# Kernel optimization log

Hardware: AMD Instinct MI355X
Metric: run time of the kernel (lower is better)

Reference implementation:

```python
import jax, jax.numpy as jnp
import numpy as np

NUM_FEATURES = 26
H1 = 24
H2 = 8
SEQ_LEN = 5
BATCH = 262144


def _lstm(x, w_ih, w_hh, b_ih, b_hh):
    """batch_first LSTM matching torch gate order (i, f, g, o).
    x: [B, T, I]; w_ih: [4H, I]; w_hh: [4H, H]; b_*: [4H].
    Returns (outputs [B, T, H], h_final [B, H])."""
    H = w_hh.shape[1]
    B = x.shape[0]
    # Precompute input contribution for all timesteps: [T, B, 4H]
    xg = jnp.einsum('bti,gi->tbg', x, w_ih) + (b_ih + b_hh)

    def step(carry, g_t):
        h, c = carry
        gates = g_t + h @ w_hh.T  # [B, 4H]
        i, f, g, o = jnp.split(gates, 4, axis=-1)
        i = jax.nn.sigmoid(i)
        f = jax.nn.sigmoid(f)
        g = jnp.tanh(g)
        o = jax.nn.sigmoid(o)
        c = f * c + i * g
        h = o * jnp.tanh(c)
        return (h, c), h

    h0 = jnp.zeros((B, H), dtype=x.dtype)
    c0 = jnp.zeros((B, H), dtype=x.dtype)
    (h_final, _), hs = jax.lax.scan(step, (h0, c0), xg)
    return jnp.transpose(hs, (1, 0, 2)), h_final


def setup_inputs() -> dict:
    key = jax.random.key(0)
    ks = jax.random.split(key, 9)
    s1 = 1.0 / np.sqrt(H1)
    s2 = 1.0 / np.sqrt(H2)
    u = lambda k, shape, s: jax.random.uniform(k, shape, jnp.float32, -s, s)
    return {
        'x': jax.random.normal(ks[0], (BATCH, SEQ_LEN, NUM_FEATURES), jnp.float32),
        'w_ih1': u(ks[1], (4 * H1, NUM_FEATURES), s1),
        'w_hh1': u(ks[2], (4 * H1, H1), s1),
        'b_ih1': u(ks[3], (4 * H1,), s1),
        'b_hh1': u(ks[4], (4 * H1,), s1),
        'w_ih2': u(ks[5], (4 * H2, H1), s2),
        'w_hh2': u(ks[6], (4 * H2, H2), s2),
        'b_ih2': u(ks[7], (4 * H2,), s2),
        'b_hh2': u(ks[8], (4 * H2,), s2),
    }


def reference(x, w_ih1, w_hh1, b_ih1, b_hh1, w_ih2, w_hh2, b_ih2, b_hh2):
    y1, _ = _lstm(x, w_ih1, w_hh1, b_ih1, b_hh1)        # [B, T, 24]
    _, h2 = _lstm(y1, w_ih2, w_hh2, b_ih2, b_hh2)        # [B, 8]
    return h2.reshape(-1, 1, H2)                          # [B, 1, 8]
```

## Files before the change

### kernel.cpp

```cpp
#include <hip/hip_runtime.h>

#define DEV_INLINE __device__ __forceinline__

constexpr int NF = 26;
constexpr int H1 = 24;
constexpr int H2 = 8;
constexpr int T  = 5;
constexpr int BPW  = 32;
constexpr int ROWU = 20;

constexpr float L2E     = 1.44269504088896f;
constexpr float TWO_L2E = 2.88539008177792f;

typedef _Float16 f16x8 __attribute__((ext_vector_type(8)));
typedef float    f32x4 __attribute__((ext_vector_type(4)));
typedef __fp16   fp16x2 __attribute__((ext_vector_type(2)));

union Q { uint4 u; f16x8 h; };

DEV_INLINE float fast_rcp(float x) { return __builtin_amdgcn_rcpf(x); }
DEV_INLINE float rcp1p(float x) { return fast_rcp(1.0f + __builtin_amdgcn_exp2f(-x)); }
DEV_INLINE float cellp(float i_, float f_, float g_, float o_, float& c) {
    const float ig = rcp1p(i_), fg = rcp1p(f_);
    const float gg = fmaf(2.0f, rcp1p(g_), -1.0f);
    const float og = rcp1p(o_);
    c = fmaf(fg, c, ig * gg);
    return og * fmaf(2.0f, rcp1p(c * TWO_L2E), -1.0f);
}
DEV_INLINE uint pkrtz(float a, float b) {
    union { uint u; fp16x2 p; } v; v.p = __builtin_amdgcn_cvt_pkrtz(a, b); return v.u;
}
DEV_INLINE float swz8(float v) {
    union { float f; int i; } a, b;
    a.f = v;
    b.i = __builtin_amdgcn_ds_swizzle(a.i, 0x201F);
    return b.f;
}


__global__ __launch_bounds__(256, 5) void lstm2_mfma(
    const float* __restrict__ x,
    const float* __restrict__ w_ih1, const float* __restrict__ w_hh1,
    const float* __restrict__ b_ih1, const float* __restrict__ b_hh1,
    const float* __restrict__ w_ih2, const float* __restrict__ w_hh2,
    const float* __restrict__ b_ih2, const float* __restrict__ b_hh2,
    float* __restrict__ out, int batch)
{
    __shared__ uint4 sW[20][64];
    __shared__ uint  sH[4][BPW * ROWU];
    __shared__ float sB1[8 * 16];
    __shared__ float sB2[4 * 16];

    const int tid = threadIdx.x;
    const int w   = tid >> 6;
    const int l   = tid & 63;
    const int q   = l >> 4;
    const int r16 = l & 15;
    const bool lo = (r16 < 8);
    const int wb  = blockIdx.x * 128 + w * BPW;

    for (int i = l; i < BPW * ROWU; i += 64) sH[w][i] = 0u;

    int row0 = wb + r16;      if (row0 > batch - 1) row0 = batch - 1;
    int row1 = wb + 16 + r16; if (row1 > batch - 1) row1 = batch - 1;
    const float* __restrict__ xp0 = x + (size_t)row0 * (T * NF) + q * 8;
    const float* __restrict__ xp1 = x + (size_t)row1 * (T * NF) + q * 8;
    const bool q3 = (q == 3);
    const float2 z2 = make_float2(0.0f, 0.0f);

    float2 xr_[2][4];
    #pragma unroll
    for (int m = 0; m < 2; ++m) {
        const float* __restrict__ p = m ? xp1 : xp0;
        xr_[m][0] = *reinterpret_cast<const float2*>(p);
        xr_[m][1] = q3 ? z2 : *reinterpret_cast<const float2*>(p + 2);
        xr_[m][2] = q3 ? z2 : *reinterpret_cast<const float2*>(p + 4);
        xr_[m][3] = q3 ? z2 : *reinterpret_cast<const float2*>(p + 6);
    }

    for (int tile = w; tile < 20; tile += 4) {
        f16x8 bf;
        if (tile < 16) {
            const int tau  = tile & 7;
            const int gate = tau >> 1, j = (tau & 1) * 16 + r16;
            const bool jv  = (j < H1);
            const int row  = gate * H1 + (jv ? j : 0);
            const bool ih  = (tile < 8);
            const float sc = (gate == 2) ? TWO_L2E : L2E;
            #pragma unroll
            for (int e = 0; e < 8; ++e) {
                const int k = q * 8 + e;
                float v = 0.0f;
                if (ih) { if (jv && k < NF) v = w_ih1[row * NF + k]; }
                else    { if (jv && k < H1) v = w_hh1[row * H1 + k]; }
                bf[e] = (_Float16)(v * sc);
            }
        } else {
            const int t2  = tile - 16;
            const bool jv = (r16 < H2);
            const int row = t2 * H2 + (jv ? r16 : 0);
            const float sc = (t2 == 2) ? TWO_L2E : L2E;
            #pragma unroll
            for (int e = 0; e < 8; ++e) {
                const int k = q * 8 + e;
                float v = 0.0f;
                if (jv) v = (k < H1) ? w_ih2[row * H1 + k] : w_hh2[row * H2 + (k - H1)];
                bf[e] = (_Float16)(v * sc);
            }
        }
        Q u; u.h = bf;
        sW[tile][l] = u.u;
    }

    if (tid < 128) {
        const int tau = tid >> 4, col = tid & 15;
        const int gate = tau >> 1, j = (tau & 1) * 16 + col;
        const bool jv = (j < H1);
        const int row = gate * H1 + (jv ? j : 0);
        const float sc = (gate == 2) ? TWO_L2E : L2E;
        sB1[tid] = jv ? (b_ih1[row] + b_hh1[row]) * sc : 0.0f;
    } else if (tid < 192) {
        const int idx = tid - 128;
        const int t2 = idx >> 4, col = idx & 15;
        const bool jv = (col < H2);
        const int row = t2 * H2 + (jv ? col : 0);
        const float sc = (t2 == 2) ? TWO_L2E : L2E;
        sB2[idx] = jv ? (b_ih2[row] + b_hh2[row]) * sc : 0.0f;
    }

    __syncthreads();

    float c1a[2][4] = {}, c1b[4] = {}, c2s[4] = {};
    const uint4* HQ = reinterpret_cast<const uint4*>(&sH[w][0]);
    _Float16*   Hh  = reinterpret_cast<_Float16*>(&sH[w][0]);

    #pragma unroll 1
    for (int t = 0; t < T; ++t) {
        Q xa[2];
        #pragma unroll
        for (int m = 0; m < 2; ++m) {
            uint4 u;
            u.x = pkrtz(xr_[m][0].x, xr_[m][0].y);
            u.y = pkrtz(xr_[m][1].x, xr_[m][1].y);
            u.z = pkrtz(xr_[m][2].x, xr_[m][2].y);
            u.w = pkrtz(xr_[m][3].x, xr_[m][3].y);
            xa[m].u = u;
        }
        if (t < T - 1) {
            #pragma unroll
            for (int m = 0; m < 2; ++m) {
                const float* __restrict__ p = (m ? xp1 : xp0) + (t + 1) * NF;
                xr_[m][0] = *reinterpret_cast<const float2*>(p);
                xr_[m][1] = q3 ? z2 : *reinterpret_cast<const float2*>(p + 2);
                xr_[m][2] = q3 ? z2 : *reinterpret_cast<const float2*>(p + 4);
                xr_[m][3] = q3 ? z2 : *reinterpret_cast<const float2*>(p + 6);
            }
        }

        Q ha[2];
        #pragma unroll
        for (int m = 0; m < 2; ++m) ha[m].u = HQ[(m * 16 + r16) * 5 + q];
        __builtin_amdgcn_sched_barrier(0);

        f32x4 acc[2][4];

        #pragma unroll
        for (int g = 0; g < 4; ++g) {
            const float b = sB1[(2 * g) * 16 + r16];
            f32x4 bv = {b, b, b, b};
            acc[0][g] = bv;
            acc[1][g] = bv;
        }
        #pragma unroll
        for (int g = 0; g < 4; ++g) {
            const int tau = 2 * g;
            Q wi, wh;
            wi.u = sW[tau][l];
            wh.u = sW[8 + tau][l];
            acc[0][g] = __builtin_amdgcn_mfma_f32_16x16x32_f16(xa[0].h, wi.h, acc[0][g], 0, 0, 0);
            acc[1][g] = __builtin_amdgcn_mfma_f32_16x16x32_f16(xa[1].h, wi.h, acc[1][g], 0, 0, 0);
            acc[0][g] = __builtin_amdgcn_mfma_f32_16x16x32_f16(ha[0].h, wh.h, acc[0][g], 0, 0, 0);
            acc[1][g] = __builtin_amdgcn_mfma_f32_16x16x32_f16(ha[1].h, wh.h, acc[1][g], 0, 0, 0);
            if (g == 1) __builtin_amdgcn_sched_barrier(0);
        }
        __builtin_amdgcn_sched_barrier(0);
        #pragma unroll
        for (int m = 0; m < 2; ++m) {
            #pragma unroll
            for (int r = 0; r < 4; ++r) {
                const int lrow = m * 16 + q * 4 + r;
                const float hv = cellp(acc[m][0][r], acc[m][1][r], acc[m][2][r], acc[m][3][r], c1a[m][r]);
                Hh[lrow * 40 + r16] = (_Float16)hv;
            }
        }
        __builtin_amdgcn_sched_barrier(0);

        #pragma unroll
        for (int g = 0; g < 4; ++g) {
            const float b = sB1[(2 * g + 1) * 16 + r16];
            f32x4 bv = {b, b, b, b};
            acc[0][g] = bv;
            acc[1][g] = bv;
        }
        #pragma unroll
        for (int g = 0; g < 4; ++g) {
            const int tau = 2 * g + 1;
            Q wi, wh;
            wi.u = sW[tau][l];
            wh.u = sW[8 + tau][l];
            acc[0][g] = __builtin_amdgcn_mfma_f32_16x16x32_f16(xa[0].h, wi.h, acc[0][g], 0, 0, 0);
            acc[1][g] = __builtin_amdgcn_mfma_f32_16x16x32_f16(xa[1].h, wi.h, acc[1][g], 0, 0, 0);
            acc[0][g] = __builtin_amdgcn_mfma_f32_16x16x32_f16(ha[0].h, wh.h, acc[0][g], 0, 0, 0);
            acc[1][g] = __builtin_amdgcn_mfma_f32_16x16x32_f16(ha[1].h, wh.h, acc[1][g], 0, 0, 0);
            if (g == 1) __builtin_amdgcn_sched_barrier(0);
        }
        __builtin_amdgcn_sched_barrier(0);
        #pragma unroll
        for (int r = 0; r < 4; ++r) {
            const float si = swz8(acc[1][0][r]);
            const float sf = swz8(acc[1][1][r]);
            const float sg = swz8(acc[1][2][r]);
            const float so = swz8(acc[1][3][r]);
            const float i_ = lo ? acc[0][0][r] : si;
            const float f_ = lo ? acc[0][1][r] : sf;
            const float g_ = lo ? acc[0][2][r] : sg;
            const float o_ = lo ? acc[0][3][r] : so;
            const float hv = cellp(i_, f_, g_, o_, c1b[r]);
            const int lrow = (lo ? 0 : 16) + q * 4 + r;
            Hh[lrow * 40 + 16 + (r16 & 7)] = (_Float16)hv;
        }
        __builtin_amdgcn_sched_barrier(0);

        Q hc[2];
        #pragma unroll
        for (int m = 0; m < 2; ++m) hc[m].u = HQ[(m * 16 + r16) * 5 + q];
        __builtin_amdgcn_sched_barrier(0);
        #pragma unroll
        for (int t2 = 0; t2 < 4; ++t2) {
            const float b = sB2[t2 * 16 + r16];
            f32x4 bv = {b, b, b, b};
            acc[0][t2] = bv;
            acc[1][t2] = bv;
        }
        #pragma unroll
        for (int t2 = 0; t2 < 4; ++t2) {
            Q wc; wc.u = sW[16 + t2][l];
            acc[0][t2] = __builtin_amdgcn_mfma_f32_16x16x32_f16(hc[0].h, wc.h, acc[0][t2], 0, 0, 0);
            acc[1][t2] = __builtin_amdgcn_mfma_f32_16x16x32_f16(hc[1].h, wc.h, acc[1][t2], 0, 0, 0);
        }
        __builtin_amdgcn_sched_barrier(0);
        #pragma unroll
        for (int r = 0; r < 4; ++r) {
            const float si = swz8(acc[1][0][r]);
            const float sf = swz8(acc[1][1][r]);
            const float sg = swz8(acc[1][2][r]);
            const float so = swz8(acc[1][3][r]);
            const float i_ = lo ? acc[0][0][r] : si;
            const float f_ = lo ? acc[0][1][r] : sf;
            const float g_ = lo ? acc[0][2][r] : sg;
            const float o_ = lo ? acc[0][3][r] : so;
            const float h2v = cellp(i_, f_, g_, o_, c2s[r]);
            const int lrow = (lo ? 0 : 16) + q * 4 + r;
            Hh[lrow * 40 + 24 + (r16 & 7)] = (_Float16)h2v;
        }
        __builtin_amdgcn_sched_barrier(0);
    }

    {
        const int erow = l >> 1, ecg = l & 1;
        const uint2 hv = *reinterpret_cast<const uint2*>(&Hh[erow * 40 + 24 + ecg * 4]);
        union { uint u; fp16x2 p; } a0, a1;
        a0.u = hv.x; a1.u = hv.y;
        const int orow = wb + erow;
        if (orow < batch) {
            float4 o = make_float4((float)a0.p[0], (float)a0.p[1],
                                   (float)a1.p[0], (float)a1.p[1]);
            *reinterpret_cast<float4*>(out + (size_t)orow * H2 + ecg * 4) = o;
        }
    }
}

extern "C" void kernel_launch(void* const* d_in, const int* in_sizes, int n_in,
                              void* d_out, int out_size, void* d_ws, size_t ws_size,
                              hipStream_t stream)
{
    const float* x     = (const float*)d_in[0];
    const float* w_ih1 = (const float*)d_in[1];
    const float* w_hh1 = (const float*)d_in[2];
    const float* b_ih1 = (const float*)d_in[3];
    const float* b_hh1 = (const float*)d_in[4];
    const float* w_ih2 = (const float*)d_in[5];
    const float* w_hh2 = (const float*)d_in[6];
    const float* b_ih2 = (const float*)d_in[7];
    const float* b_hh2 = (const float*)d_in[8];
    float* out = (float*)d_out;

    const int batch = in_sizes[0] / (T * NF);
    const int block = 256;
    const int grid  = (batch + 127) / 128;
    lstm2_mfma<<<grid, block, 0, stream>>>(x, w_ih1, w_hh1, b_ih1, b_hh1,
                                           w_ih2, w_hh2, b_ih2, b_hh2,
                                           out, batch);
}
```

Measured before the change: 80.24 us.

## Keep x in packed fp16 across steps, move prefetch later, use DPP swap

The input for the current timestep is now carried in packed fp16 registers (xcur), so the next step's global loads are issued after the first layer-1 gate half and converted at the end of the step. This keeps only 16 packed values live during the first MFMA block instead of 32 floats, and holds the prefetched loads in flight for a shorter window. The cross-half lane swap moves from ds_swizzle to a DPP row_shr-style move, which avoids the LDS crossbar. The launch-bounds occupancy hint drops from 5 to 4 waves to give the compiler more registers. The risks are less latency hiding for the x loads and lower occupancy.

```diff
diff --git a/kernel.cpp b/kernel.cpp
--- a/kernel.cpp
+++ b/kernel.cpp
@@ -33,12 +33,12 @@
 DEV_INLINE float swz8(float v) {
     union { float f; int i; } a, b;
     a.f = v;
-    b.i = __builtin_amdgcn_ds_swizzle(a.i, 0x201F);
+    b.i = __builtin_amdgcn_mov_dpp(a.i, 0x128, 0xf, 0xf, true);
     return b.f;
 }
 
 
-__global__ __launch_bounds__(256, 5) void lstm2_mfma(
+__global__ __launch_bounds__(256, 4) void lstm2_mfma(
     const float* __restrict__ x,
     const float* __restrict__ w_ih1, const float* __restrict__ w_hh1,
     const float* __restrict__ b_ih1, const float* __restrict__ b_hh1,
@@ -68,14 +68,14 @@
     const bool q3 = (q == 3);
     const float2 z2 = make_float2(0.0f, 0.0f);
 
-    float2 xr_[2][4];
+    float2 xr0[2][4];
     #pragma unroll
     for (int m = 0; m < 2; ++m) {
         const float* __restrict__ p = m ? xp1 : xp0;
-        xr_[m][0] = *reinterpret_cast<const float2*>(p);
-        xr_[m][1] = q3 ? z2 : *reinterpret_cast<const float2*>(p + 2);
-        xr_[m][2] = q3 ? z2 : *reinterpret_cast<const float2*>(p + 4);
-        xr_[m][3] = q3 ? z2 : *reinterpret_cast<const float2*>(p + 6);
+        xr0[m][0] = *reinterpret_cast<const float2*>(p);
+        xr0[m][1] = q3 ? z2 : *reinterpret_cast<const float2*>(p + 2);
+        xr0[m][2] = q3 ? z2 : *reinterpret_cast<const float2*>(p + 4);
+        xr0[m][3] = q3 ? z2 : *reinterpret_cast<const float2*>(p + 6);
     }
 
     for (int tile = w; tile < 20; tile += 4) {
@@ -130,22 +130,62 @@
 
     __syncthreads();
 
+    Q xcur[2];
+    #pragma unroll
+    for (int m = 0; m < 2; ++m) {
+        uint4 u;
+        u.x = pkrtz(xr0[m][0].x, xr0[m][0].y);
+        u.y = pkrtz(xr0[m][1].x, xr0[m][1].y);
+        u.z = pkrtz(xr0[m][2].x, xr0[m][2].y);
+        u.w = pkrtz(xr0[m][3].x, xr0[m][3].y);
+        xcur[m].u = u;
+    }
+
     float c1a[2][4] = {}, c1b[4] = {}, c2s[4] = {};
     const uint4* HQ = reinterpret_cast<const uint4*>(&sH[w][0]);
     _Float16*   Hh  = reinterpret_cast<_Float16*>(&sH[w][0]);
 
     #pragma unroll 1
     for (int t = 0; t < T; ++t) {
-        Q xa[2];
+        Q ha[2];
+        #pragma unroll
+        for (int m = 0; m < 2; ++m) ha[m].u = HQ[(m * 16 + r16) * 5 + q];
+        __builtin_amdgcn_sched_barrier(0);
+
+        f32x4 acc[2][4];
+
+        #pragma unroll
+        for (int g = 0; g < 4; ++g) {
+            const float b = sB1[(2 * g) * 16 + r16];
+            f32x4 bv = {b, b, b, b};
+            acc[0][g] = bv;
+            acc[1][g] = bv;
+        }
+        #pragma unroll
+        for (int g = 0; g < 4; ++g) {
+            const int tau = 2 * g;
+            Q wi, wh;
+            wi.u = sW[tau][l];
+            wh.u = sW[8 + tau][l];
+            acc[0][g] = __builtin_amdgcn_mfma_f32_16x16x32_f16(xcur[0].h, wi.h, acc[0][g], 0, 0, 0);
+            acc[1][g] = __builtin_amdgcn_mfma_f32_16x16x32_f16(xcur[1].h, wi.h, acc[1][g], 0, 0, 0);
+            acc[0][g] = __builtin_amdgcn_mfma_f32_16x16x32_f16(ha[0].h, wh.h, acc[0][g], 0, 0, 0);
+            acc[1][g] = __builtin_amdgcn_mfma_f32_16x16x32_f16(ha[1].h, wh.h, acc[1][g], 0, 0, 0);
+            if (g == 1) __builtin_amdgcn_sched_barrier(0);
+        }
+        __builtin_amdgcn_sched_barrier(0);
         #pragma unroll
         for (int m = 0; m < 2; ++m) {
-            uint4 u;
-            u.x = pkrtz(xr_[m][0].x, xr_[m][0].y);
-            u.y = pkrtz(xr_[m][1].x, xr_[m][1].y);
-            u.z = pkrtz(xr_[m][2].x, xr_[m][2].y);
-            u.w = pkrtz(xr_[m][3].x, xr_[m][3].y);
-            xa[m].u = u;
-        }
+            #pragma unroll
+            for (int r = 0; r < 4; ++r) {
+                const int lrow = m * 16 + q * 4 + r;
+                const float hv = cellp(acc[m][0][r], acc[m][1][r], acc[m][2][r], acc[m][3][r], c1a[m][r]);
+                Hh[lrow * 40 + r16] = (_Float16)hv;
+            }
+        }
+        __builtin_amdgcn_sched_barrier(0);
+
+        float2 xr_[2][4];
         if (t < T - 1) {
             #pragma unroll
             for (int m = 0; m < 2; ++m) {
@@ -157,44 +197,6 @@
             }
         }
 
-        Q ha[2];
-        #pragma unroll
-        for (int m = 0; m < 2; ++m) ha[m].u = HQ[(m * 16 + r16) * 5 + q];
-        __builtin_amdgcn_sched_barrier(0);
-
-        f32x4 acc[2][4];
-
-        #pragma unroll
-        for (int g = 0; g < 4; ++g) {
-            const float b = sB1[(2 * g) * 16 + r16];
-            f32x4 bv = {b, b, b, b};
-            acc[0][g] = bv;
-            acc[1][g] = bv;
-        }
-        #pragma unroll
-        for (int g = 0; g < 4; ++g) {
-            const int tau = 2 * g;
-            Q wi, wh;
-            wi.u = sW[tau][l];
-            wh.u = sW[8 + tau][l];
-            acc[0][g] = __builtin_amdgcn_mfma_f32_16x16x32_f16(xa[0].h, wi.h, acc[0][g], 0, 0, 0);
-            acc[1][g] = __builtin_amdgcn_mfma_f32_16x16x32_f16(xa[1].h, wi.h, acc[1][g], 0, 0, 0);
-            acc[0][g] = __builtin_amdgcn_mfma_f32_16x16x32_f16(ha[0].h, wh.h, acc[0][g], 0, 0, 0);
-            acc[1][g] = __builtin_amdgcn_mfma_f32_16x16x32_f16(ha[1].h, wh.h, acc[1][g], 0, 0, 0);
-            if (g == 1) __builtin_amdgcn_sched_barrier(0);
-        }
-        __builtin_amdgcn_sched_barrier(0);
-        #pragma unroll
-        for (int m = 0; m < 2; ++m) {
-            #pragma unroll
-            for (int r = 0; r < 4; ++r) {
-                const int lrow = m * 16 + q * 4 + r;
-                const float hv = cellp(acc[m][0][r], acc[m][1][r], acc[m][2][r], acc[m][3][r], c1a[m][r]);
-                Hh[lrow * 40 + r16] = (_Float16)hv;
-            }
-        }
-        __builtin_amdgcn_sched_barrier(0);
-
         #pragma unroll
         for (int g = 0; g < 4; ++g) {
             const float b = sB1[(2 * g + 1) * 16 + r16];
@@ -208,8 +210,8 @@
             Q wi, wh;
             wi.u = sW[tau][l];
             wh.u = sW[8 + tau][l];
-            acc[0][g] = __builtin_amdgcn_mfma_f32_16x16x32_f16(xa[0].h, wi.h, acc[0][g], 0, 0, 0);
-            acc[1][g] = __builtin_amdgcn_mfma_f32_16x16x32_f16(xa[1].h, wi.h, acc[1][g], 0, 0, 0);
+            acc[0][g] = __builtin_amdgcn_mfma_f32_16x16x32_f16(xcur[0].h, wi.h, acc[0][g], 0, 0, 0);
+            acc[1][g] = __builtin_amdgcn_mfma_f32_16x16x32_f16(xcur[1].h, wi.h, acc[1][g], 0, 0, 0);
             acc[0][g] = __builtin_amdgcn_mfma_f32_16x16x32_f16(ha[0].h, wh.h, acc[0][g], 0, 0, 0);
             acc[1][g] = __builtin_amdgcn_mfma_f32_16x16x32_f16(ha[1].h, wh.h, acc[1][g], 0, 0, 0);
             if (g == 1) __builtin_amdgcn_sched_barrier(0);
@@ -262,6 +264,18 @@
             const float h2v = cellp(i_, f_, g_, o_, c2s[r]);
             const int lrow = (lo ? 0 : 16) + q * 4 + r;
             Hh[lrow * 40 + 24 + (r16 & 7)] = (_Float16)h2v;
+        }
+
+        if (t < T - 1) {
+            #pragma unroll
+            for (int m = 0; m < 2; ++m) {
+                uint4 u;
+                u.x = pkrtz(xr_[m][0].x, xr_[m][0].y);
+                u.y = pkrtz(xr_[m][1].x, xr_[m][1].y);
+                u.z = pkrtz(xr_[m][2].x, xr_[m][2].y);
+                u.w = pkrtz(xr_[m][3].x, xr_[m][3].y);
+                xcur[m].u = u;
+            }
         }
         __builtin_amdgcn_sched_barrier(0);
     }
```

Measured after the change: 74.58 us. 1.08x faster.
